# Kernel tuning notes

Measured on AMD Instinct MI355X. Metric: run time of the kernel, lower is better.

## Reference

```python
import jax, jax.numpy as jnp
import numpy as np

NB_NEIGHBORS = 8


def _euclidean_distances(X):
    # X: (n, d); pairwise distances between rows, clamped at 0 before sqrt.
    sq = jnp.sum(jnp.square(X), axis=1)  # (n,)
    d = -2.0 * (X @ X.T) + sq[None, :] + sq[:, None]
    return jnp.sqrt(jnp.maximum(d, 0.0))


def setup_inputs() -> dict:
    key = jax.random.key(0)
    k1, k2 = jax.random.split(key)
    B, C, F, D3 = 64, 4, 8192, 1
    d_coord = 64
    inputs = jax.random.normal(k1, (B, C, F, D3), dtype=jnp.float32)
    coordinates = jax.random.normal(k2, (d_coord, 1, F), dtype=jnp.float32)
    return {"inputs": inputs, "coordinates": coordinates}


def reference(inputs, coordinates):
    # coordinates: (d, 1, F) -> crd: (d, F); features are columns.
    d, _, F = coordinates.shape
    crd = coordinates.reshape(d, F)
    dist = _euclidean_distances(crd.T)  # (F, F) distances between features
    # top-k smallest distances per feature (indices of nearest features)
    _, idx = jax.lax.top_k(-dist, NB_NEIGHBORS)  # (F, K)
    # Original loop: first slot hardcoded to feature 0, then idx[0,1:],
    # then idx[f,:] for f >= 1. Flatten into one gather index vector.
    flat_idx = jnp.concatenate(
        [jnp.zeros((1,), dtype=idx.dtype), idx[0, 1:], idx[1:].reshape(-1)]
    )  # (F*K,)
    # Single fused gather along the feature axis: (B, C, F*K, D3)
    return jnp.take(inputs, flat_idx, axis=2)
```

## Files before the change

kernel.cpp:

```cpp
#include <hip/hip_runtime.h>

#define F      8192
#define KD     64
#define NB     8
#define WROWS  32
#define MKEEP  16
#define JQ     4
#define CPR    64
#define NROUND ((F / JQ) / CPR)
#define CAP    96
#define MARGIN 0.25f

typedef unsigned long long u64;
typedef unsigned short ushort_t;
typedef __attribute__((ext_vector_type(8))) _Float16 f16x8;
typedef __attribute__((ext_vector_type(4))) float f32x4;

__device__ __forceinline__ u64 pack64(float d, int j) {
    return ((u64)__float_as_uint(d) << 32) | (unsigned)j;
}

template<int CTRL>
__device__ __forceinline__ u64 dpp_u64(u64 x) {
    unsigned lo = (unsigned)x, hi = (unsigned)(x >> 32);
    lo = (unsigned)__builtin_amdgcn_update_dpp(0, (int)lo, CTRL, 0xF, 0xF, true);
    hi = (unsigned)__builtin_amdgcn_update_dpp(0, (int)hi, CTRL, 0xF, 0xF, true);
    return ((u64)hi << 32) | lo;
}
__device__ __forceinline__ u64 swap_xor1(u64 x) { return dpp_u64<0xB1>(x); }
__device__ __forceinline__ u64 swap_xor2(u64 x) { return dpp_u64<0x4E>(x); }
__device__ __forceinline__ u64 swap_xor4(u64 x, int n) {
    u64 shr = dpp_u64<0x114>(x);
    u64 shl = dpp_u64<0x104>(x);
    return (n & 4) ? shr : shl;
}
__device__ __forceinline__ u64 swap_xor8(u64 x, int n) {
    u64 shr = dpp_u64<0x118>(x);
    u64 shl = dpp_u64<0x108>(x);
    return (n & 8) ? shr : shl;
}
__device__ __forceinline__ u64 swap_mirror(u64 x) { return dpp_u64<0x140>(x); }

#define CEK(x, J, K, SW)                                                      \
    { u64 px = SW; bool wmin = ((n & (J)) == 0) == ((n & (K)) == 0);          \
      x = (wmin == (px < x)) ? px : x; }
#define CEA(L, J, SW)                                                         \
    { u64 pl = SW; bool wmin = ((n & (J)) == 0);                              \
      L = (wmin == (pl < L)) ? pl : L; }
#define SORT16(x)                                                             \
    CEK(x, 1, 2,  swap_xor1(x))                                               \
    CEK(x, 2, 4,  swap_xor2(x))    CEK(x, 1, 4,  swap_xor1(x))                \
    CEK(x, 4, 8,  swap_xor4(x,n))  CEK(x, 2, 8,  swap_xor2(x))                \
    CEK(x, 1, 8,  swap_xor1(x))                                               \
    CEK(x, 8, 16, swap_xor8(x,n))  CEK(x, 4, 16, swap_xor4(x,n))              \
    CEK(x, 2, 16, swap_xor2(x))    CEK(x, 1, 16, swap_xor1(x))

__global__ __launch_bounds__(256) void prep_kernel(const float* __restrict__ crd,
                                                   float* __restrict__ sq,
                                                   ushort_t* __restrict__ XtH,
                                                   float* __restrict__ Xt32) {
    const int f = blockIdx.x * 256 + threadIdx.x;
    float acc = 0.f;
#pragma unroll
    for (int kb = 0; kb < 8; ++kb) {
        ushort_t hb[8];
        float    xv[8];
#pragma unroll
        for (int u = 0; u < 8; ++u) {
            int k = kb * 8 + u;
            float x = crd[k * F + f];
            acc = fmaf(x, x, acc);
            hb[u] = __builtin_bit_cast(ushort_t, (_Float16)x);
            xv[u] = x;
        }
        *(uint4*)&XtH[(size_t)f * KD + kb * 8] = *(const uint4*)hb;
        *(float4*)&Xt32[(size_t)f * KD + kb * 8]     = *(const float4*)&xv[0];
        *(float4*)&Xt32[(size_t)f * KD + kb * 8 + 4] = *(const float4*)&xv[4];
    }
    sq[f] = acc;
}

__global__ __launch_bounds__(256, 4) void knn_mfma(const ushort_t* __restrict__ XtH,
                                                   const float* __restrict__ sq,
                                                   u64* __restrict__ part) {
    __shared__ u64 buf[WROWS][CAP + 1];
    __shared__ u64 lst[WROWS][MKEEP + 1];
    __shared__ __align__(16) float thr[WROWS];
    __shared__ int cnt[WROWS];

    const int tid  = threadIdx.x;
    const int wave = tid >> 6;
    const int tx   = tid & 63;
    const int quad = tx >> 4;
    const int n    = tx & 15;
    const int blockRow = (blockIdx.x >> 2) * WROWS;
    const int jq    = blockIdx.x & 3;
    const int jbase = jq * (F / JQ);

    if (tid < WROWS) { cnt[tid] = 0; thr[tid] = __int_as_float(0x7f800000); }
#pragma unroll
    for (int e = tid; e < WROWS * MKEEP; e += 256) lst[e >> 4][e & 15] = ~0ULL;
    __syncthreads();

    const size_t a0 = (size_t)(blockRow + n) * KD + quad * 8;
    const size_t a1 = (size_t)(blockRow + 16 + n) * KD + quad * 8;
    const f16x8 a0h0 = *(const f16x8*)(XtH + a0), a0h1 = *(const f16x8*)(XtH + a0 + 32);
    const f16x8 a1h0 = *(const f16x8*)(XtH + a1), a1h1 = *(const f16x8*)(XtH + a1 + 32);
    const f32x4 sqi0 = *(const f32x4*)&sq[blockRow + quad * 4];
    const f32x4 sqi1 = *(const f32x4*)&sq[blockRow + 16 + quad * 4];
    f32x4 pre0, pre1;
#pragma unroll
    for (int r = 0; r < 4; ++r) { pre0[r] = -__int_as_float(0x7f800000);
                                  pre1[r] = -__int_as_float(0x7f800000); }

    const int laneCol = wave * 16 + n;

#define LOADB(H0, H1, SJ, RND)                                                \
    {   int jc = jbase + (RND) * CPR + laneCol;                               \
        size_t bo = (size_t)jc * KD + quad * 8;                               \
        H0 = *(const f16x8*)(XtH + bo); H1 = *(const f16x8*)(XtH + bo + 32);  \
        SJ = sq[jc]; }

#define MFMABODY(H0, H1)                                                      \
        f32x4 za0 = {0,0,0,0}, za1 = {0,0,0,0};                               \
        za0 = __builtin_amdgcn_mfma_f32_16x16x32_f16(a0h0, H0, za0, 0, 0, 0); \
        za0 = __builtin_amdgcn_mfma_f32_16x16x32_f16(a0h1, H1, za0, 0, 0, 0); \
        za1 = __builtin_amdgcn_mfma_f32_16x16x32_f16(a1h0, H0, za1, 0, 0, 0); \
        za1 = __builtin_amdgcn_mfma_f32_16x16x32_f16(a1h1, H1, za1, 0, 0, 0);

#define PROCESS0(H0, H1, SJ, RND)                                             \
    {   MFMABODY(H0, H1)                                                      \
        const int jc = jbase + (RND) * CPR + laneCol;                         \
        _Pragma("unroll")                                                     \
        for (int r = 0; r < 4; ++r) {                                         \
            float d0 = fmaxf((sqi0[r] + SJ) - 2.f * za0[r], 0.f);             \
            buf[quad * 4 + r][laneCol] = pack64(d0, jc);                      \
            float d1 = fmaxf((sqi1[r] + SJ) - 2.f * za1[r], 0.f);             \
            buf[16 + quad * 4 + r][laneCol] = pack64(d1, jc);                 \
        } }

#define PROCESS(H0, H1, SJ, RND)                                              \
    {   MFMABODY(H0, H1)                                                      \
        const int jc = jbase + (RND) * CPR + laneCol;                         \
        const float h = 0.5f * SJ;                                            \
        _Pragma("unroll")                                                     \
        for (int r = 0; r < 4; ++r) {                                         \
            float dot = za0[r];                                               \
            if (dot >= pre0[r] + h) {                                         \
                float d = fmaxf((sqi0[r] + SJ) - 2.f * dot, 0.f);             \
                int row = quad * 4 + r;                                       \
                int q = atomicAdd(&cnt[row], 1);                              \
                if (q < CAP) buf[row][q] = pack64(d, jc);                     \
            }                                                                 \
            dot = za1[r];                                                     \
            if (dot >= pre1[r] + h) {                                         \
                float d = fmaxf((sqi1[r] + SJ) - 2.f * dot, 0.f);             \
                int row = 16 + quad * 4 + r;                                  \
                int q = atomicAdd(&cnt[row], 1);                              \
                if (q < CAP) buf[row][q] = pack64(d, jc);                     \
            }                                                                 \
        } }

#define FOLD(R0)                                                              \
    {   __syncthreads();                                                      \
        _Pragma("unroll")                                                     \
        for (int p = 0; p < 2; ++p) {                                         \
            const int row = p * 16 + wave * 4 + quad;                         \
            u64 Lv = lst[row][n];                                             \
            const u64 tmax = __shfl(Lv, (tx & 48) | 15, 64);                  \
            const int nn = (R0) ? CPR : min(cnt[row], CAP);                   \
            for (int ii = 0; ii < nn; ii += 16) {                             \
                u64 x = (ii + n < nn) ? buf[row][ii + n] : ~0ULL;             \
                u64 bal = __ballot(x < tmax);                                 \
                if ((unsigned short)(bal >> (quad * 16)) == 0) continue;      \
                SORT16(x)                                                     \
                u64 xr = swap_mirror(x);               \
                Lv = (xr < Lv) ? xr : Lv;                    \
                CEA(Lv, 8, swap_xor8(Lv, n))                                  \
                CEA(Lv, 4, swap_xor4(Lv, n))                                  \
                CEA(Lv, 2, swap_xor2(Lv))                                     \
                CEA(Lv, 1, swap_xor1(Lv))                                     \
            }                                                                 \
            lst[row][n] = Lv;                                                 \
            if (n == NB - 1) thr[row] = __uint_as_float((unsigned)(Lv >> 32)) + MARGIN; \
            if (n == 0) cnt[row] = 0;                                         \
        }                                                                     \
        __syncthreads();                                                      \
        {   f32x4 t0 = *(const f32x4*)&thr[quad * 4];                         \
            f32x4 t1 = *(const f32x4*)&thr[16 + quad * 4];                    \
            _Pragma("unroll")                                                 \
            for (int r = 0; r < 4; ++r) {                                     \
                pre0[r] = 0.5f * (sqi0[r] - t0[r]);                           \
                pre1[r] = 0.5f * (sqi1[r] - t1[r]);                           \
            } } }

    f16x8 B0h0, B0h1, B1h0, B1h1;
    float B0sj, B1sj;
    LOADB(B0h0, B0h1, B0sj, 0)
    LOADB(B1h0, B1h1, B1sj, 1)

    PROCESS0(B0h0, B0h1, B0sj, 0)
    LOADB(B0h0, B0h1, B0sj, 2)
    FOLD(1)
    PROCESS(B1h0, B1h1, B1sj, 1)
    LOADB(B1h0, B1h1, B1sj, 3)
    FOLD(0)

    for (int rr = 2; rr < NROUND; rr += 2) {
        PROCESS(B0h0, B0h1, B0sj, rr)
        if (rr + 2 < NROUND) LOADB(B0h0, B0h1, B0sj, rr + 2)
        PROCESS(B1h0, B1h1, B1sj, rr + 1)
        if (rr + 3 < NROUND) LOADB(B1h0, B1h1, B1sj, rr + 3)
        if (((rr + 1) & (rr + 2)) == 0) FOLD(0)
    }

#pragma unroll
    for (int e = tid; e < WROWS * MKEEP; e += 256) {
        int rrw = e >> 4, ss = e & 15;
        part[((size_t)jq * F + blockRow + rrw) * MKEEP + ss] = lst[rrw][ss];
    }
#undef LOADB
#undef MFMABODY
#undef PROCESS0
#undef PROCESS
#undef FOLD
}

__global__ __launch_bounds__(256) void recheck_kernel(const float* __restrict__ Xt32,
                                                      const float* __restrict__ sq,
                                                      const u64* __restrict__ part,
                                                      int* __restrict__ knn) {
    __shared__ float A_s[4][KD];
    const int tid = threadIdx.x;
    const int rl = tid >> 6, tx = tid & 63;
    const int i = blockIdx.x * 4 + rl;

    A_s[tid >> 6][tid & 63] = Xt32[(size_t)(blockIdx.x * 4 + (tid >> 6)) * KD + (tid & 63)];
    __syncthreads();

    u64 pc = part[((size_t)(tx >> 4) * F + i) * MKEEP + (tx & 15)];
    int j = (int)(pc & 0xffffffffu);

    const float4* b4 = (const float4*)(Xt32 + (size_t)j * KD);
    float acc = 0.f;
#pragma unroll
    for (int kk = 0; kk < KD / 4; ++kk) {
        float4 b = b4[kk];
        const float* a = &A_s[rl][kk * 4];
        acc = fmaf(a[0], b.x, acc);
        acc = fmaf(a[1], b.y, acc);
        acc = fmaf(a[2], b.z, acc);
        acc = fmaf(a[3], b.w, acc);
    }
    float d = fmaxf((sq[i] + sq[j]) - 2.f * acc, 0.f);
    u64 mine = pack64(d, j);

    int myout = 0;
#pragma unroll
    for (int s = 0; s < NB; ++s) {
        u64 m = mine;
#pragma unroll
        for (int off = 32; off >= 1; off >>= 1) {
            u64 o = __shfl_xor(m, off, 64);
            if (o < m) m = o;
        }
        if (mine == m) mine = ~0ULL;
        if (tx == s) myout = (int)(m & 0xffffffffu);
    }
    if (tx < NB) knn[(size_t)i * NB + tx] = myout;
}

__global__ __launch_bounds__(512) void gather_kernel(const float* __restrict__ inp,
                                                     const int* __restrict__ knn,
                                                     float* __restrict__ out) {
    __shared__ float row[F];
    const int bc    = blockIdx.x >> 2;
    const int chunk = blockIdx.x & 3;
    const int tid   = threadIdx.x;

    const float4* in4  = (const float4*)(inp + (size_t)bc * F);
    float4*       row4 = (float4*)row;
#pragma unroll
    for (int i = 0; i < (F / 4) / 512; ++i) row4[i * 512 + tid] = in4[i * 512 + tid];
    __syncthreads();

    const int4* kn4 = (const int4*)knn;
    float4*     ou4 = (float4*)(out + (size_t)bc * (F * NB));

#pragma unroll
    for (int i = 0; i < 8; ++i) {
        int e = chunk * 4096 + i * 512 + tid;
        int4 idx = kn4[e];
        if (e == 0) idx.x = 0;
        float4 o;
        o.x = row[idx.x]; o.y = row[idx.y]; o.z = row[idx.z]; o.w = row[idx.w];
        ou4[e] = o;
    }
}

extern "C" void kernel_launch(void* const* d_in, const int* in_sizes, int n_in,
                              void* d_out, int out_size, void* d_ws, size_t ws_size,
                              hipStream_t stream) {
    const float* inp = (const float*)d_in[0];
    const float* crd = (const float*)d_in[1];
    float* out = (float*)d_out;

    ushort_t* XtH  = (ushort_t*)d_ws;
    float*    Xt32 = (float*)((char*)d_ws + (2u << 20));
    float*    sq   = (float*)((char*)d_ws + (4u << 20));
    int*      knn  = (int*)((char*)d_ws + (4u << 20) + (1u << 15));
    u64*      part = (u64*)((char*)d_ws + (5u << 20));

    prep_kernel<<<F / 256, 256, 0, stream>>>(crd, sq, XtH, Xt32);
    knn_mfma<<<(F / WROWS) * JQ, 256, 0, stream>>>(XtH, sq, part);
    recheck_kernel<<<F / 4, 256, 0, stream>>>(Xt32, sq, part, knn);
    gather_kernel<<<256 * 4, 512, 0, stream>>>(inp, knn, out);
}
```

Before: 163.5 us.

## Halve rows per block in KNN MFMA kernel to double block count

Reduces each block's tile of query rows from 32 to 16, so each wave runs one 16-row MFMA strip instead of two, and raises the launch-bounds occupancy hint to 8 blocks per CU. The aim is more blocks, lower register and LDS use per block, and better latency hiding. In exchange, every column tile of XtH is loaded by twice as many blocks, which doubles B-operand global traffic and halves reuse per load. The fold step now handles one row group per wave instead of two.

Measured after the change: 185.9 us. 1.14x slower.

```diff
diff --git a/kernel.cpp b/kernel.cpp
--- a/kernel.cpp
+++ b/kernel.cpp
@@ -3,7 +3,7 @@
 #define F      8192
 #define KD     64
 #define NB     8
-#define WROWS  32
+#define WROWS  16
 #define MKEEP  16
 #define JQ     4
 #define CPR    64
@@ -80,7 +80,7 @@
     sq[f] = acc;
 }
 
-__global__ __launch_bounds__(256, 4) void knn_mfma(const ushort_t* __restrict__ XtH,
+__global__ __launch_bounds__(256, 8) void knn_mfma(const ushort_t* __restrict__ XtH,
                                                    const float* __restrict__ sq,
                                                    u64* __restrict__ part) {
     __shared__ u64 buf[WROWS][CAP + 1];
@@ -98,20 +98,15 @@
     const int jbase = jq * (F / JQ);
 
     if (tid < WROWS) { cnt[tid] = 0; thr[tid] = __int_as_float(0x7f800000); }
-#pragma unroll
-    for (int e = tid; e < WROWS * MKEEP; e += 256) lst[e >> 4][e & 15] = ~0ULL;
+    if (tid < WROWS * MKEEP) lst[tid >> 4][tid & 15] = ~0ULL;
     __syncthreads();
 
     const size_t a0 = (size_t)(blockRow + n) * KD + quad * 8;
-    const size_t a1 = (size_t)(blockRow + 16 + n) * KD + quad * 8;
     const f16x8 a0h0 = *(const f16x8*)(XtH + a0), a0h1 = *(const f16x8*)(XtH + a0 + 32);
-    const f16x8 a1h0 = *(const f16x8*)(XtH + a1), a1h1 = *(const f16x8*)(XtH + a1 + 32);
     const f32x4 sqi0 = *(const f32x4*)&sq[blockRow + quad * 4];
-    const f32x4 sqi1 = *(const f32x4*)&sq[blockRow + 16 + quad * 4];
-    f32x4 pre0, pre1;
-#pragma unroll
-    for (int r = 0; r < 4; ++r) { pre0[r] = -__int_as_float(0x7f800000);
-                                  pre1[r] = -__int_as_float(0x7f800000); }
+    f32x4 pre0;
+#pragma unroll
+    for (int r = 0; r < 4; ++r) pre0[r] = -__int_as_float(0x7f800000);
 
     const int laneCol = wave * 16 + n;
 
@@ -122,11 +117,9 @@
         SJ = sq[jc]; }
 
 #define MFMABODY(H0, H1)                                                      \
-        f32x4 za0 = {0,0,0,0}, za1 = {0,0,0,0};                               \
+        f32x4 za0 = {0,0,0,0};                                                \
         za0 = __builtin_amdgcn_mfma_f32_16x16x32_f16(a0h0, H0, za0, 0, 0, 0); \
-        za0 = __builtin_amdgcn_mfma_f32_16x16x32_f16(a0h1, H1, za0, 0, 0, 0); \
-        za1 = __builtin_amdgcn_mfma_f32_16x16x32_f16(a1h0, H0, za1, 0, 0, 0); \
-        za1 = __builtin_amdgcn_mfma_f32_16x16x32_f16(a1h1, H1, za1, 0, 0, 0);
+        za0 = __builtin_amdgcn_mfma_f32_16x16x32_f16(a0h1, H1, za0, 0, 0, 0);
 
 #define PROCESS0(H0, H1, SJ, RND)                                             \
     {   MFMABODY(H0, H1)                                                      \
@@ -135,8 +128,6 @@
         for (int r = 0; r < 4; ++r) {                                         \
             float d0 = fmaxf((sqi0[r] + SJ) - 2.f * za0[r], 0.f);             \
             buf[quad * 4 + r][laneCol] = pack64(d0, jc);                      \
-            float d1 = fmaxf((sqi1[r] + SJ) - 2.f * za1[r], 0.f);             \
-            buf[16 + quad * 4 + r][laneCol] = pack64(d1, jc);                 \
         } }
 
 #define PROCESS(H0, H1, SJ, RND)                                              \
@@ -152,20 +143,11 @@
                 int q = atomicAdd(&cnt[row], 1);                              \
                 if (q < CAP) buf[row][q] = pack64(d, jc);                     \
             }                                                                 \
-            dot = za1[r];                                                     \
-            if (dot >= pre1[r] + h) {                                         \
-                float d = fmaxf((sqi1[r] + SJ) - 2.f * dot, 0.f);             \
-                int row = 16 + quad * 4 + r;                                  \
-                int q = atomicAdd(&cnt[row], 1);                              \
-                if (q < CAP) buf[row][q] = pack64(d, jc);                     \
-            }                                                                 \
         } }
 
 #define FOLD(R0)                                                              \
     {   __syncthreads();                                                      \
-        _Pragma("unroll")                                                     \
-        for (int p = 0; p < 2; ++p) {                                         \
-            const int row = p * 16 + wave * 4 + quad;                         \
+        {   const int row = wave * 4 + quad;                                  \
             u64 Lv = lst[row][n];                                             \
             const u64 tmax = __shfl(Lv, (tx & 48) | 15, 64);                  \
             const int nn = (R0) ? CPR : min(cnt[row], CAP);                   \
@@ -187,12 +169,9 @@
         }                                                                     \
         __syncthreads();                                                      \
         {   f32x4 t0 = *(const f32x4*)&thr[quad * 4];                         \
-            f32x4 t1 = *(const f32x4*)&thr[16 + quad * 4];                    \
             _Pragma("unroll")                                                 \
-            for (int r = 0; r < 4; ++r) {                                     \
-                pre0[r] = 0.5f * (sqi0[r] - t0[r]);                           \
-                pre1[r] = 0.5f * (sqi1[r] - t1[r]);                           \
-            } } }
+            for (int r = 0; r < 4; ++r) pre0[r] = 0.5f * (sqi0[r] - t0[r]);   \
+        } }
 
     f16x8 B0h0, B0h1, B1h0, B1h1;
     float B0sj, B1sj;
@@ -214,9 +193,8 @@
         if (((rr + 1) & (rr + 2)) == 0) FOLD(0)
     }
 
-#pragma unroll
-    for (int e = tid; e < WROWS * MKEEP; e += 256) {
-        int rrw = e >> 4, ss = e & 15;
+    {
+        int rrw = tid >> 4, ss = tid & 15;
         part[((size_t)jq * F + blockRow + rrw) * MKEEP + ss] = lst[rrw][ss];
     }
 #undef LOADB
```
